# Kernel optimization log

Hardware: AMD Instinct MI355X
Metric: run time of the kernel (lower is better)

The kernel has to match this reference:

```python
import jax, jax.numpy as jnp
import numpy as np

NUM_CLASSES = 21
THRESH = 0.5
NEG_POS = 3
VAR0, VAR1 = 0.1, 0.2


def point_form(boxes):
    # center form (cx,cy,w,h) -> corner form (x1,y1,x2,y2)
    return jnp.concatenate([boxes[:, :2] - boxes[:, 2:] / 2,
                            boxes[:, :2] + boxes[:, 2:] / 2], axis=1)


def jaccard(a, b):
    # a: [N,4] corner form, b: [P,4] corner form -> IoU [N,P]
    lt = jnp.maximum(a[:, None, :2], b[None, :, :2])
    rb = jnp.minimum(a[:, None, 2:], b[None, :, 2:])
    wh = jnp.clip(rb - lt, 0.0)
    inter = wh[..., 0] * wh[..., 1]
    area_a = (a[:, 2] - a[:, 0]) * (a[:, 3] - a[:, 1])
    area_b = (b[:, 2] - b[:, 0]) * (b[:, 3] - b[:, 1])
    return inter / (area_a[:, None] + area_b[None, :] - inter)


def match_one(truths, labels, priors):
    # truths: [N,4] corner form, labels: [N] int, priors: [P,4] center form
    ov = jaccard(truths, point_form(priors))            # [N,P]
    best_prior_idx = jnp.argmax(ov, axis=1)             # [N] best prior per truth
    best_truth_ov = jnp.max(ov, axis=0)                 # [P]
    best_truth_idx = jnp.argmax(ov, axis=0)             # [P]
    # ensure each truth keeps its best prior
    best_truth_ov = best_truth_ov.at[best_prior_idx].set(2.0)
    best_truth_idx = best_truth_idx.at[best_prior_idx].set(
        jnp.arange(truths.shape[0], dtype=best_truth_idx.dtype))
    matches = truths[best_truth_idx]                    # [P,4]
    conf = labels[best_truth_idx] + 1                   # [P]
    conf = jnp.where(best_truth_ov < THRESH, 0, conf)
    # encode
    g_cxcy = ((matches[:, :2] + matches[:, 2:]) / 2 - priors[:, :2]) / (VAR0 * priors[:, 2:])
    g_wh = jnp.log((matches[:, 2:] - matches[:, :2]) / priors[:, 2:]) / VAR1
    return jnp.concatenate([g_cxcy, g_wh], axis=1), conf


def setup_inputs() -> dict:
    key = jax.random.key(0)
    k1, k2, k3, k4, k5, k6, k7 = jax.random.split(key, 7)
    B, P, C, N = 64, 24564, NUM_CLASSES, 16
    loc_data = jax.random.normal(k1, (B, P, 4), dtype=jnp.float32)
    conf_data = jax.random.normal(k2, (B, P, C), dtype=jnp.float32)
    # priors: valid center-form boxes
    ctr = 0.05 + 0.9 * jax.random.uniform(k3, (P, 2), dtype=jnp.float32)
    pwh = 0.05 + 0.25 * jax.random.uniform(k4, (P, 2), dtype=jnp.float32)
    priors = jnp.concatenate([ctr, pwh], axis=1)
    # truths: valid corner-form boxes
    xy1 = 0.7 * jax.random.uniform(k5, (B, N, 2), dtype=jnp.float32)
    twh = 0.05 + 0.2 * jax.random.uniform(k6, (B, N, 2), dtype=jnp.float32)
    truths = jnp.concatenate([xy1, xy1 + twh], axis=2)
    labels = jax.random.randint(k7, (B, N), 0, 20, dtype=jnp.int32)
    return {"loc_data": loc_data, "conf_data": conf_data, "priors": priors,
            "truths": truths, "labels": labels}


def reference(loc_data, conf_data, priors, truths, labels):
    B, P, C = conf_data.shape
    loc_t, conf_t = jax.vmap(lambda t, l: match_one(t, l, priors))(truths, labels)
    pos = conf_t > 0                                     # [B,P]

    # localization smooth-L1, summed over positives
    diff = loc_data - loc_t
    ad = jnp.abs(diff)
    sl1 = jnp.where(ad < 1.0, 0.5 * diff * diff, ad - 0.5)
    loss_l = jnp.sum(sl1 * pos[..., None].astype(loc_data.dtype))

    # per-prior CE = logsumexp - logit at matched class
    lse = jax.nn.logsumexp(conf_data, axis=2)            # [B,P]
    gathered = jnp.take_along_axis(conf_data, conf_t[..., None].astype(jnp.int32), axis=2)[..., 0]
    loss_c_all = lse - gathered

    # hard-negative mining via double argsort rank (pos zeroed first)
    loss_c_mine = jnp.where(pos, 0.0, loss_c_all)
    idx_rank = jnp.argsort(jnp.argsort(-loss_c_mine, axis=1), axis=1)
    num_pos = jnp.sum(pos, axis=1, keepdims=True)        # [B,1]
    num_neg = jnp.minimum(NEG_POS * num_pos, P - 1)
    neg = idx_rank < num_neg

    mask = pos | neg
    loss_c = jnp.sum(jnp.where(mask, loss_c_all, 0.0))

    n = jnp.sum(num_pos).astype(loc_data.dtype)
    return loss_l / n, loss_c / n
```

## Files before the change

### kernel.cpp

```cpp
#include <hip/hip_runtime.h>
#include <cstdint>
#include <cstddef>

#define B_ 64
#define P_ 24564
#define C_ 21
#define N_ 16
#define NPB_ 24
#define NPL_ 96
#define THRESH_ 0.5f


__device__ inline unsigned long long shfl_down_u64(unsigned long long v, int off) {
    unsigned lo = (unsigned)v, hi = (unsigned)(v >> 32);
    lo = __shfl_down(lo, off);
    hi = __shfl_down(hi, off);
    return ((unsigned long long)hi << 32) | lo;
}

__device__ inline void async_copy16(const float* g, float* l) {
    __builtin_amdgcn_global_load_lds(
        (const __attribute__((address_space(1))) void*)g,
        (__attribute__((address_space(3))) void*)l, 16, 0, 0);
}

__device__ inline float sl1_encode(float4 ld, float4 pr,
                                   float tx1, float ty1, float tx2, float ty2) {
    float gcx = ((tx1 + tx2) * 0.5f - pr.x) / (0.1f * pr.z);
    float gcy = ((ty1 + ty2) * 0.5f - pr.y) / (0.1f * pr.w);
    float gw  = __logf((tx2 - tx1) / pr.z) / 0.2f;
    float gh  = __logf((ty2 - ty1) / pr.w) / 0.2f;
    float g[4] = {gcx, gcy, gw, gh};
    float l[4] = {ld.x, ld.y, ld.z, ld.w};
    float s = 0.0f;
#pragma unroll
    for (int i = 0; i < 4; i++) {
        float d = l[i] - g[i];
        float ad = fabsf(d);
        s += (ad < 1.0f) ? 0.5f * d * d : ad - 0.5f;
    }
    return s;
}


__global__ __launch_bounds__(256, 4) void
kM_match(const float* __restrict__ priors,
         const float* __restrict__ truths,
         uint32_t* __restrict__ matchw,
         unsigned long long* __restrict__ part_key) {
    int b = blockIdx.y, bx = blockIdx.x, t = threadIdx.x;
    int wid = t >> 6, lane = t & 63;
    __shared__ float tr[N_ * 4];
    __shared__ unsigned skey[N_ * 256];
    if (t < N_ * 4) tr[t] = truths[b * N_ * 4 + t];
    __syncthreads();

    int p0 = bx * 1024 + 4 * t;
    bool valid = p0 < P_;

    float px1[4], py1[4], px2[4], py2[4], ap[4];
#pragma unroll
    for (int r = 0; r < 4; r++) {
        float4 pr = valid ? ((const float4*)priors)[p0 + r]
                          : make_float4(0.5f, 0.5f, 0.1f, 0.1f);
        px1[r] = pr.x - pr.z * 0.5f; py1[r] = pr.y - pr.w * 0.5f;
        px2[r] = pr.x + pr.z * 0.5f; py2[r] = pr.y + pr.w * 0.5f;
        ap[r] = (px2[r] - px1[r]) * (py2[r] - py1[r]);
    }

    float best[4] = {-1.0f, -1.0f, -1.0f, -1.0f};
    int bn[4] = {0, 0, 0, 0};
#pragma unroll
    for (int n = 0; n < N_; n++) {
        float tx1 = tr[n * 4 + 0], ty1 = tr[n * 4 + 1];
        float tx2 = tr[n * 4 + 2], ty2 = tr[n * 4 + 3];
        float at = (tx2 - tx1) * (ty2 - ty1);
        float tbi = -1.0f;
        int tbr = 0;
#pragma unroll
        for (int r = 0; r < 4; r++) {
            float lx = fmaxf(tx1, px1[r]), ly = fmaxf(ty1, py1[r]);
            float rx = fminf(tx2, px2[r]), ry = fminf(ty2, py2[r]);
            float w = fmaxf(rx - lx, 0.0f), h = fmaxf(ry - ly, 0.0f);
            float inter = w * h;
            float iou = inter / (at + ap[r] - inter);
            if (iou > best[r]) { best[r] = iou; bn[r] = n; }
            if (iou > tbi) { tbi = iou; tbr = r; }
        }
        skey[n * 256 + t] = valid
            ? ((__float_as_uint(tbi) << 2) | (unsigned)(3 - tbr)) : 0u;
    }

    if (valid) {
        uint32_t w = 0;
#pragma unroll
        for (int r = 0; r < 4; r++) {
            uint32_t byte = (uint32_t)bn[r] | ((best[r] < THRESH_) ? 0u : 0x10u);
            w |= byte << (8 * r);
        }
        matchw[(size_t)b * (P_ / 4) + (p0 >> 2)] = w;
    }

    __syncthreads();
#pragma unroll
    for (int i = 0; i < 4; i++) {
        int n = wid + 4 * i;
        unsigned long long bk = 0ull;
#pragma unroll
        for (int q = 0; q < 4; q++) {
            int tt = lane + 64 * q;
            unsigned k32 = skey[n * 256 + tt];
            unsigned long long v = ((unsigned long long)k32 << 32) |
                                   (unsigned)~(unsigned)tt;
            bk = (v > bk) ? v : bk;
        }
        for (int off = 32; off; off >>= 1) {
            unsigned long long o = shfl_down_u64(bk, off);
            bk = (o > bk) ? o : bk;
        }
        if (lane == 0) {
            int twin = (int)~(unsigned)(bk & 0xFFFFFFFFull);
            unsigned k32 = (unsigned)(bk >> 32);
            int pwin = bx * 1024 + 4 * twin + (3 - (int)(k32 & 3u));
            part_key[(size_t)(b * NPB_ + bx) * N_ + n] =
                ((unsigned long long)(k32 >> 2) << 32) | (unsigned)~(unsigned)pwin;
        }
    }
}

__global__ __launch_bounds__(256, 6) void
kL_lse(const float* __restrict__ loc,
       const float* __restrict__ conf,
       const float* __restrict__ priors,
       const float* __restrict__ truths,
       const int* __restrict__ labels,
       const uint32_t* __restrict__ matchw,
       float* __restrict__ mine,
       float* __restrict__ part_ll,
       float* __restrict__ part_pce,
       int* __restrict__ part_np) {
    int b = blockIdx.y, bx = blockIdx.x, t = threadIdx.x;
    int wid = t >> 6, lane = t & 63;
    __shared__ float scf[256 * C_];
    __shared__ float tr[N_ * 4];
    __shared__ int lb[N_];
    __shared__ float sll[4], spc[4];
    __shared__ int snp[4];
    if (t < N_ * 4) tr[t] = truths[b * N_ * 4 + t];
    if (t < N_) lb[t] = labels[b * N_ + t];

    int base_p = bx * 256;
    int nvalid = min(256, P_ - base_p);
    int maxf4 = (nvalid * C_) >> 2;
    const float* gtile = conf + ((size_t)b * P_ + base_p) * C_;

    for (int k = wid; k < 21; k += 4) {
        int f4 = k * 64 + lane;
        int s4 = (f4 < maxf4) ? f4 : (maxf4 - 1);
        async_copy16(gtile + (size_t)s4 * 4, scf + k * 256);
    }
    __syncthreads();

    int p0 = base_p + t;
    bool valid = t < nvalid;

    float ll = 0.0f, pce = 0.0f;
    int np = 0;
    if (valid) {
        uint32_t mwv = matchw[(size_t)b * (P_ / 4) + (p0 >> 2)];
        uint32_t byte = (mwv >> (8 * (p0 & 3))) & 0xFFu;
        int bti = (int)(byte & 15u);
        int pos = (int)(byte >> 4);
        int cls = pos ? (lb[bti] + 1) : 0;

        float ssum = 0.0f;
#pragma unroll
        for (int i = 0; i < 21; i++) ssum += __expf(scf[t * 21 + i]);
        float g = scf[t * 21 + cls];
        float lca = fmaxf(__logf(ssum) - g, 0.0f);

        mine[(size_t)b * P_ + p0] = pos ? 0.0f : lca;

        if (pos) {
            np = 1;
            pce = lca;
            float4 prr = ((const float4*)priors)[p0];
            float4 ld = ((const float4*)loc)[(size_t)b * P_ + p0];
            ll = sl1_encode(ld, prr, tr[bti * 4 + 0], tr[bti * 4 + 1],
                            tr[bti * 4 + 2], tr[bti * 4 + 3]);
        }
    }

    for (int off = 32; off; off >>= 1) {
        ll += __shfl_down(ll, off);
        pce += __shfl_down(pce, off);
        np += __shfl_down(np, off);
    }
    if (lane == 0) { sll[wid] = ll; spc[wid] = pce; snp[wid] = np; }
    __syncthreads();
    if (t == 0) {
        float a = 0.0f, cc = 0.0f;
        int q = 0;
        for (int i = 0; i < 4; i++) { a += sll[i]; cc += spc[i]; q += snp[i]; }
        part_ll[b * NPL_ + bx] = a;
        part_pce[b * NPL_ + bx] = cc;
        part_np[b * NPL_ + bx] = q;
    }
}

__global__ __launch_bounds__(1024) void
kB_batch(const float* __restrict__ loc,
         const float* __restrict__ conf,
         const float* __restrict__ priors,
         const float* __restrict__ truths,
         const int* __restrict__ labels,
         const float* __restrict__ mine,
         const float* __restrict__ part_ll,
         const float* __restrict__ part_pce,
         const int* __restrict__ part_np,
         const unsigned long long* __restrict__ part_key,
         double* __restrict__ bll,
         double* __restrict__ bpc,
         int* __restrict__ bnp) {
    int b = blockIdx.x, t = threadIdx.x, wid = t >> 6, lane = t & 63;
    __shared__ float tr[N_ * 4];
    __shared__ int lb[N_];
    __shared__ int sp[N_];
    __shared__ float sdll, sdpce, sll_s, spc_s;
    __shared__ int sdnp, snp_s;
    __shared__ int scnt[16];
    __shared__ unsigned sT;
    __shared__ float wsum[16];
    __shared__ int wcgt[16];

    if (t < N_ * 4) tr[t] = truths[b * N_ * 4 + t];
    if (t < N_) lb[t] = labels[b * N_ + t];
    if (t == 0) { sdll = 0.f; sdpce = 0.f; sdnp = 0; sll_s = 0.f; spc_s = 0.f; snp_s = 0; }
    if (t < N_) {
        unsigned long long best = 0ull;
        for (int i = 0; i < NPB_; i++) {
            unsigned long long k = part_key[(size_t)(b * NPB_ + i) * N_ + t];
            best = (k > best) ? k : best;
        }
        sp[t] = (int)~(unsigned)(best & 0xFFFFFFFFull);
    }
    __syncthreads();
    if (t < NPL_) {
        atomicAdd(&sll_s, part_ll[b * NPL_ + t]);
        atomicAdd(&spc_s, part_pce[b * NPL_ + t]);
        atomicAdd(&snp_s, part_np[b * NPL_ + t]);
    }
    if (t < N_) {
        int p = sp[t];
        bool last = true;
        for (int n = t + 1; n < N_; n++) if (sp[n] == p) last = false;
        if (last) {
            int nf = t;
            float4 pr = ((const float4*)priors)[p];
            float px1 = pr.x - pr.z * 0.5f, py1 = pr.y - pr.w * 0.5f;
            float px2 = pr.x + pr.z * 0.5f, py2 = pr.y + pr.w * 0.5f;
            float ap = (px2 - px1) * (py2 - py1);
            float best = -1.0f;
            int bti = 0;
            for (int n = 0; n < N_; n++) {
                float tx1 = tr[n * 4], ty1 = tr[n * 4 + 1];
                float tx2 = tr[n * 4 + 2], ty2 = tr[n * 4 + 3];
                float at = (tx2 - tx1) * (ty2 - ty1);
                float lx = fmaxf(tx1, px1), ly = fmaxf(ty1, py1);
                float rx = fminf(tx2, px2), ry = fminf(ty2, py2);
                float w = fmaxf(rx - lx, 0.0f), h = fmaxf(ry - ly, 0.0f);
                float inter = w * h;
                float iou = inter / (at + ap - inter);
                if (iou > best) { best = iou; bti = n; }
            }
            int pos_old = (best >= THRESH_) ? 1 : 0;
            const float* cp = conf + ((size_t)b * P_ + p) * C_;
            float x[C_];
            float ssum = 0.0f;
            for (int j = 0; j < C_; j++) { x[j] = cp[j]; ssum += __expf(x[j]); }
            float lse = __logf(ssum);
            float4 ld = ((const float4*)loc)[(size_t)b * P_ + p];
            float dll = sl1_encode(ld, pr, tr[nf * 4], tr[nf * 4 + 1],
                                   tr[nf * 4 + 2], tr[nf * 4 + 3]);
            float dpce = lse - x[lb[nf] + 1];
            int dnp = 1 - pos_old;
            if (pos_old) {
                dll -= sl1_encode(ld, pr, tr[bti * 4], tr[bti * 4 + 1],
                                  tr[bti * 4 + 2], tr[bti * 4 + 3]);
                dpce -= lse - x[lb[bti] + 1];
            }
            atomicAdd(&sdll, dll);
            atomicAdd(&sdpce, dpce);
            atomicAdd(&sdnp, dnp);
        }
    }

    unsigned omask = 0;
#pragma unroll
    for (int n = 0; n < N_; n++) {
        int p = sp[n];
        if ((p & 1023) == t) omask |= 1u << (p >> 10);
    }
    const float* v = mine + (size_t)b * P_;
    int nel = (t < (P_ - 23 * 1024)) ? 24 : 23;
    float xv[24];
#pragma unroll
    for (int i = 0; i < 24; i++) {
        float x = 0.0f;
        if (i < nel) x = v[t + (i << 10)];
        if ((omask >> i) & 1) x = 0.0f;
        xv[i] = x;
    }
    __syncthreads();
    int np = snp_s + sdnp;
    int k = np * 3;
    if (k > P_ - 1) k = P_ - 1;

    unsigned T = 0u;
    for (int bpos = 30; bpos >= 0; bpos--) {
        unsigned cand = T | (1u << bpos);
        int c = 0;
#pragma unroll
        for (int i = 0; i < 24; i++)
            if (__float_as_uint(xv[i]) >= cand) c++;
        for (int off = 32; off; off >>= 1) c += __shfl_down(c, off);
        if (lane == 0) scnt[wid] = c;
        __syncthreads();
        if (t == 0) {
            int tot = 0;
            for (int i = 0; i < 16; i++) tot += scnt[i];
            sT = (tot >= k) ? cand : T;
        }
        __syncthreads();
        T = sT;
    }

    float psum = 0.0f;
    int cgt = 0;
#pragma unroll
    for (int i = 0; i < 24; i++) {
        if (__float_as_uint(xv[i]) > T) { psum += xv[i]; cgt++; }
    }
    for (int off = 32; off; off >>= 1) {
        psum += __shfl_down(psum, off);
        cgt += __shfl_down(cgt, off);
    }
    if (lane == 0) { wsum[wid] = psum; wcgt[wid] = cgt; }
    __syncthreads();
    if (t == 0) {
        float s2 = 0.0f;
        int cg = 0;
        for (int i = 0; i < 16; i++) { s2 += wsum[i]; cg += wcgt[i]; }
        int skrem = k - cg;
        double tot = (double)s2 + (double)skrem * (double)__uint_as_float(T);
        bll[b] = (double)(sll_s + sdll);
        bpc[b] = (double)(spc_s + sdpce) + tot;
        bnp[b] = np;
    }
}

__global__ void kC_final(const double* __restrict__ bll,
                         const double* __restrict__ bpc,
                         const int* __restrict__ bnp,
                         float* __restrict__ out) {
    int t = threadIdx.x;
    double a = bll[t], c = bpc[t];
    int n = bnp[t];
    for (int off = 32; off; off >>= 1) {
        a += __shfl_down(a, off);
        c += __shfl_down(c, off);
        n += __shfl_down(n, off);
    }
    if (t == 0) {
        double dn = (double)n;
        out[0] = (float)(a / dn);
        out[1] = (float)(c / dn);
    }
}


extern "C" void kernel_launch(void* const* d_in, const int* in_sizes, int n_in,
                              void* d_out, int out_size, void* d_ws, size_t ws_size,
                              hipStream_t stream) {
    const float* loc    = (const float*)d_in[0];
    const float* conf   = (const float*)d_in[1];
    const float* priors = (const float*)d_in[2];
    const float* truths = (const float*)d_in[3];
    const int*   labels = (const int*)d_in[4];
    float* out = (float*)d_out;

    char* ws = (char*)d_ws;
    unsigned long long* part_key = (unsigned long long*)(ws);
    float*  part_ll  = (float*)(ws + 196608);
    float*  part_pce = (float*)(ws + 221184);
    int*    part_np  = (int*)(ws + 245760);
    double* bll      = (double*)(ws + 270336);
    double* bpc      = (double*)(ws + 270848);
    int*    bnp      = (int*)(ws + 271360);
    float*  mine     = (float*)(ws + 294912);
    uint32_t* matchw = (uint32_t*)(ws + 6583296);

    hipLaunchKernelGGL(kM_match, dim3(NPB_, B_), dim3(256), 0, stream,
                       priors, truths, matchw, part_key);
    hipLaunchKernelGGL(kL_lse, dim3(NPL_, B_), dim3(256), 0, stream,
                       loc, conf, priors, truths, labels, matchw,
                       mine, part_ll, part_pce, part_np);
    hipLaunchKernelGGL(kB_batch, dim3(B_), dim3(1024), 0, stream,
                       loc, conf, priors, truths, labels, mine,
                       part_ll, part_pce, part_np, part_key, bll, bpc, bnp);
    hipLaunchKernelGGL(kC_final, dim3(1), dim3(64), 0, stream, bll, bpc, bnp, out);
}
```

Before: 279.1 us.

## Fuse prior matching into LSE kernel, drop match word buffer

Merges the matching kernel into the per-prior log-sum-exp kernel, so each block computes IoU for its own 256 priors while the conf tile is loading asynchronously. This removes one launch and the matchw global round-trip. Per-truth best-prior keys are now produced per 256-prior block (96 partials instead of 24), and the batch kernel reduces them with 256 threads and a shared atomicMax. The cost is more partial keys to reduce, plus truths read from global inside the loop instead of shared memory.

```diff
diff --git a/kernel.cpp b/kernel.cpp
--- a/kernel.cpp
+++ b/kernel.cpp
@@ -6,7 +6,6 @@
 #define P_ 24564
 #define C_ 21
 #define N_ 16
-#define NPB_ 24
 #define NPL_ 96
 #define THRESH_ 0.5f
 
@@ -44,64 +43,61 @@
 
 
 __global__ __launch_bounds__(256, 4) void
-kM_match(const float* __restrict__ priors,
+kF_fused(const float* __restrict__ loc,
+         const float* __restrict__ conf,
+         const float* __restrict__ priors,
          const float* __restrict__ truths,
-         uint32_t* __restrict__ matchw,
+         const int* __restrict__ labels,
+         float* __restrict__ mine,
+         float* __restrict__ part_ll,
+         float* __restrict__ part_pce,
+         int* __restrict__ part_np,
          unsigned long long* __restrict__ part_key) {
     int b = blockIdx.y, bx = blockIdx.x, t = threadIdx.x;
     int wid = t >> 6, lane = t & 63;
-    __shared__ float tr[N_ * 4];
+    __shared__ float scf[256 * C_];
     __shared__ unsigned skey[N_ * 256];
-    if (t < N_ * 4) tr[t] = truths[b * N_ * 4 + t];
-    __syncthreads();
-
-    int p0 = bx * 1024 + 4 * t;
-    bool valid = p0 < P_;
-
-    float px1[4], py1[4], px2[4], py2[4], ap[4];
-#pragma unroll
-    for (int r = 0; r < 4; r++) {
-        float4 pr = valid ? ((const float4*)priors)[p0 + r]
-                          : make_float4(0.5f, 0.5f, 0.1f, 0.1f);
-        px1[r] = pr.x - pr.z * 0.5f; py1[r] = pr.y - pr.w * 0.5f;
-        px2[r] = pr.x + pr.z * 0.5f; py2[r] = pr.y + pr.w * 0.5f;
-        ap[r] = (px2[r] - px1[r]) * (py2[r] - py1[r]);
-    }
-
-    float best[4] = {-1.0f, -1.0f, -1.0f, -1.0f};
-    int bn[4] = {0, 0, 0, 0};
+    __shared__ int lb[N_];
+    __shared__ float sll[4], spc[4];
+    __shared__ int snp[4];
+
+    int base_p = bx * 256;
+    int nvalid = min(256, P_ - base_p);
+    int maxf4 = (nvalid * C_) >> 2;
+    const float* gtile = conf + ((size_t)b * P_ + base_p) * C_;
+
+    for (int k = wid; k < 21; k += 4) {
+        int f4 = k * 64 + lane;
+        int s4 = (f4 < maxf4) ? f4 : (maxf4 - 1);
+        async_copy16(gtile + (size_t)s4 * 4, scf + k * 256);
+    }
+    if (t < N_) lb[t] = labels[b * N_ + t];
+
+    int p0 = base_p + t;
+    bool valid = t < nvalid;
+    float4 pr = ((const float4*)priors)[valid ? p0 : base_p];
+    float px1 = pr.x - pr.z * 0.5f, py1 = pr.y - pr.w * 0.5f;
+    float px2 = pr.x + pr.z * 0.5f, py2 = pr.y + pr.w * 0.5f;
+    float ap = (px2 - px1) * (py2 - py1);
+
+    float best = -1.0f;
+    int bn = 0;
 #pragma unroll
     for (int n = 0; n < N_; n++) {
-        float tx1 = tr[n * 4 + 0], ty1 = tr[n * 4 + 1];
-        float tx2 = tr[n * 4 + 2], ty2 = tr[n * 4 + 3];
-        float at = (tx2 - tx1) * (ty2 - ty1);
-        float tbi = -1.0f;
-        int tbr = 0;
-#pragma unroll
-        for (int r = 0; r < 4; r++) {
-            float lx = fmaxf(tx1, px1[r]), ly = fmaxf(ty1, py1[r]);
-            float rx = fminf(tx2, px2[r]), ry = fminf(ty2, py2[r]);
-            float w = fmaxf(rx - lx, 0.0f), h = fmaxf(ry - ly, 0.0f);
-            float inter = w * h;
-            float iou = inter / (at + ap[r] - inter);
-            if (iou > best[r]) { best[r] = iou; bn[r] = n; }
-            if (iou > tbi) { tbi = iou; tbr = r; }
-        }
-        skey[n * 256 + t] = valid
-            ? ((__float_as_uint(tbi) << 2) | (unsigned)(3 - tbr)) : 0u;
-    }
-
-    if (valid) {
-        uint32_t w = 0;
-#pragma unroll
-        for (int r = 0; r < 4; r++) {
-            uint32_t byte = (uint32_t)bn[r] | ((best[r] < THRESH_) ? 0u : 0x10u);
-            w |= byte << (8 * r);
-        }
-        matchw[(size_t)b * (P_ / 4) + (p0 >> 2)] = w;
-    }
-
-    __syncthreads();
+        float4 tb = ((const float4*)truths)[b * N_ + n];
+        float at = (tb.z - tb.x) * (tb.w - tb.y);
+        float lx = fmaxf(tb.x, px1), ly = fmaxf(tb.y, py1);
+        float rx = fminf(tb.z, px2), ry = fminf(tb.w, py2);
+        float w = fmaxf(rx - lx, 0.0f), h = fmaxf(ry - ly, 0.0f);
+        float inter = w * h;
+        float iou = inter / (at + ap - inter);
+        if (iou > best) { best = iou; bn = n; }
+        skey[n * 256 + t] = valid ? __float_as_uint(iou) : 0u;
+    }
+    int pos = (valid && best >= THRESH_) ? 1 : 0;
+
+    __syncthreads();
+
 #pragma unroll
     for (int i = 0; i < 4; i++) {
         int n = wid + 4 * i;
@@ -121,58 +117,16 @@
         if (lane == 0) {
             int twin = (int)~(unsigned)(bk & 0xFFFFFFFFull);
             unsigned k32 = (unsigned)(bk >> 32);
-            int pwin = bx * 1024 + 4 * twin + (3 - (int)(k32 & 3u));
-            part_key[(size_t)(b * NPB_ + bx) * N_ + n] =
-                ((unsigned long long)(k32 >> 2) << 32) | (unsigned)~(unsigned)pwin;
-        }
-    }
-}
-
-__global__ __launch_bounds__(256, 6) void
-kL_lse(const float* __restrict__ loc,
-       const float* __restrict__ conf,
-       const float* __restrict__ priors,
-       const float* __restrict__ truths,
-       const int* __restrict__ labels,
-       const uint32_t* __restrict__ matchw,
-       float* __restrict__ mine,
-       float* __restrict__ part_ll,
-       float* __restrict__ part_pce,
-       int* __restrict__ part_np) {
-    int b = blockIdx.y, bx = blockIdx.x, t = threadIdx.x;
-    int wid = t >> 6, lane = t & 63;
-    __shared__ float scf[256 * C_];
-    __shared__ float tr[N_ * 4];
-    __shared__ int lb[N_];
-    __shared__ float sll[4], spc[4];
-    __shared__ int snp[4];
-    if (t < N_ * 4) tr[t] = truths[b * N_ * 4 + t];
-    if (t < N_) lb[t] = labels[b * N_ + t];
-
-    int base_p = bx * 256;
-    int nvalid = min(256, P_ - base_p);
-    int maxf4 = (nvalid * C_) >> 2;
-    const float* gtile = conf + ((size_t)b * P_ + base_p) * C_;
-
-    for (int k = wid; k < 21; k += 4) {
-        int f4 = k * 64 + lane;
-        int s4 = (f4 < maxf4) ? f4 : (maxf4 - 1);
-        async_copy16(gtile + (size_t)s4 * 4, scf + k * 256);
-    }
-    __syncthreads();
-
-    int p0 = base_p + t;
-    bool valid = t < nvalid;
+            int pwin = base_p + twin;
+            part_key[(size_t)(b * NPL_ + bx) * N_ + n] =
+                ((unsigned long long)k32 << 32) | (unsigned)~(unsigned)pwin;
+        }
+    }
 
     float ll = 0.0f, pce = 0.0f;
     int np = 0;
     if (valid) {
-        uint32_t mwv = matchw[(size_t)b * (P_ / 4) + (p0 >> 2)];
-        uint32_t byte = (mwv >> (8 * (p0 & 3))) & 0xFFu;
-        int bti = (int)(byte & 15u);
-        int pos = (int)(byte >> 4);
-        int cls = pos ? (lb[bti] + 1) : 0;
-
+        int cls = pos ? (lb[bn] + 1) : 0;
         float ssum = 0.0f;
 #pragma unroll
         for (int i = 0; i < 21; i++) ssum += __expf(scf[t * 21 + i]);
@@ -184,10 +138,9 @@
         if (pos) {
             np = 1;
             pce = lca;
-            float4 prr = ((const float4*)priors)[p0];
             float4 ld = ((const float4*)loc)[(size_t)b * P_ + p0];
-            ll = sl1_encode(ld, prr, tr[bti * 4 + 0], tr[bti * 4 + 1],
-                            tr[bti * 4 + 2], tr[bti * 4 + 3]);
+            float4 tb = ((const float4*)truths)[b * N_ + bn];
+            ll = sl1_encode(ld, pr, tb.x, tb.y, tb.z, tb.w);
         }
     }
 
@@ -225,6 +178,7 @@
     int b = blockIdx.x, t = threadIdx.x, wid = t >> 6, lane = t & 63;
     __shared__ float tr[N_ * 4];
     __shared__ int lb[N_];
+    __shared__ unsigned long long skmax[N_];
     __shared__ int sp[N_];
     __shared__ float sdll, sdpce, sll_s, spc_s;
     __shared__ int sdnp, snp_s;
@@ -234,22 +188,26 @@
     __shared__ int wcgt[16];
 
     if (t < N_ * 4) tr[t] = truths[b * N_ * 4 + t];
-    if (t < N_) lb[t] = labels[b * N_ + t];
+    if (t < N_) { lb[t] = labels[b * N_ + t]; skmax[t] = 0ull; }
     if (t == 0) { sdll = 0.f; sdpce = 0.f; sdnp = 0; sll_s = 0.f; spc_s = 0.f; snp_s = 0; }
-    if (t < N_) {
-        unsigned long long best = 0ull;
-        for (int i = 0; i < NPB_; i++) {
-            unsigned long long k = part_key[(size_t)(b * NPB_ + i) * N_ + t];
-            best = (k > best) ? k : best;
-        }
-        sp[t] = (int)~(unsigned)(best & 0xFFFFFFFFull);
-    }
-    __syncthreads();
+    __syncthreads();
+    if (t < 256) {
+        int n = t & 15, j = t >> 4;
+        unsigned long long bk = 0ull;
+        for (int i = j; i < NPL_; i += 16) {
+            unsigned long long k = part_key[(size_t)(b * NPL_ + i) * N_ + n];
+            bk = (k > bk) ? k : bk;
+        }
+        atomicMax(&skmax[n], bk);
+    }
     if (t < NPL_) {
         atomicAdd(&sll_s, part_ll[b * NPL_ + t]);
         atomicAdd(&spc_s, part_pce[b * NPL_ + t]);
         atomicAdd(&snp_s, part_np[b * NPL_ + t]);
     }
+    __syncthreads();
+    if (t < N_) sp[t] = (int)~(unsigned)(skmax[t] & 0xFFFFFFFFull);
+    __syncthreads();
     if (t < N_) {
         int p = sp[t];
         bool last = true;
@@ -391,20 +349,17 @@
 
     char* ws = (char*)d_ws;
     unsigned long long* part_key = (unsigned long long*)(ws);
-    float*  part_ll  = (float*)(ws + 196608);
-    float*  part_pce = (float*)(ws + 221184);
-    int*    part_np  = (int*)(ws + 245760);
-    double* bll      = (double*)(ws + 270336);
-    double* bpc      = (double*)(ws + 270848);
-    int*    bnp      = (int*)(ws + 271360);
-    float*  mine     = (float*)(ws + 294912);
-    uint32_t* matchw = (uint32_t*)(ws + 6583296);
-
-    hipLaunchKernelGGL(kM_match, dim3(NPB_, B_), dim3(256), 0, stream,
-                       priors, truths, matchw, part_key);
-    hipLaunchKernelGGL(kL_lse, dim3(NPL_, B_), dim3(256), 0, stream,
-                       loc, conf, priors, truths, labels, matchw,
-                       mine, part_ll, part_pce, part_np);
+    float*  part_ll  = (float*)(ws + 786432);
+    float*  part_pce = (float*)(ws + 811008);
+    int*    part_np  = (int*)(ws + 835584);
+    double* bll      = (double*)(ws + 860160);
+    double* bpc      = (double*)(ws + 860672);
+    int*    bnp      = (int*)(ws + 861184);
+    float*  mine     = (float*)(ws + 1048576);
+
+    hipLaunchKernelGGL(kF_fused, dim3(NPL_, B_), dim3(256), 0, stream,
+                       loc, conf, priors, truths, labels,
+                       mine, part_ll, part_pce, part_np, part_key);
     hipLaunchKernelGGL(kB_batch, dim3(B_), dim3(1024), 0, stream,
                        loc, conf, priors, truths, labels, mine,
                        part_ll, part_pce, part_np, part_key, bll, bpc, bnp);
```

New measurement: 258.9 us. 1.08x faster.
